# Kernel tuning notes

Hardware: AMD Instinct MI355X
Metric: run time of the kernel (lower is better)

The kernel has to match this reference:

```python
import jax, jax.numpy as jnp
import numpy as np

D_IN, D_H1, D_H2, D_OUT = 24, 64, 128, 64

def setup_inputs() -> dict:
    key = jax.random.key(0)
    ks = jax.random.split(key, 7)
    B, L = 256, 2048
    input_data = jax.random.normal(ks[0], (B, L, D_IN), dtype=jnp.float32)
    s = lambda fan_in: 1.0 / np.sqrt(fan_in)
    W1 = jax.random.uniform(ks[1], (D_IN, D_H1), minval=-s(D_IN), maxval=s(D_IN), dtype=jnp.float32)
    b1 = jax.random.uniform(ks[2], (D_H1,), minval=-s(D_IN), maxval=s(D_IN), dtype=jnp.float32)
    W2 = jax.random.uniform(ks[3], (D_H1, D_H2), minval=-s(D_H1), maxval=s(D_H1), dtype=jnp.float32)
    b2 = jax.random.uniform(ks[4], (D_H2,), minval=-s(D_H1), maxval=s(D_H1), dtype=jnp.float32)
    W3 = jax.random.uniform(ks[5], (D_H2, D_OUT), minval=-s(D_H2), maxval=s(D_H2), dtype=jnp.float32)
    b3 = jax.random.uniform(ks[6], (D_OUT,), minval=-s(D_H2), maxval=s(D_H2), dtype=jnp.float32)
    return {"input_data": input_data, "W1": W1, "b1": b1, "W2": W2, "b2": b2, "W3": W3, "b3": b3, "batch_size": 256}

def reference(input_data, W1, b1, W2, b2, W3, b3, batch_size):
    # Vectorized equivalent of the per-(batch,line) MLP loop:
    # three Linear+ReLU layers applied to every [24]-dim vector.
    h = jax.nn.relu(jnp.einsum('bli,ij->blj', input_data, W1) + b1)
    h = jax.nn.relu(jnp.einsum('bli,ij->blj', h, W2) + b2)
    out = jax.nn.relu(jnp.einsum('bli,ij->blj', h, W3) + b3)  # [B, L, 64]
    return out
```

## Files before the change

### kernel.cpp

```cpp
#include <hip/hip_runtime.h>

typedef float f32x4 __attribute__((ext_vector_type(4)));
typedef short s16x8 __attribute__((ext_vector_type(8)));
typedef unsigned int u32;
typedef unsigned int u32x4 __attribute__((ext_vector_type(4)));
typedef unsigned short u16;

#define DIN 24
#define DH1 64
#define DH2 128
#define DOUT 64

static __device__ __forceinline__ u16 f2bf(float f) {
    u32 u = __builtin_bit_cast(u32, f);
    u += 0x7FFFu + ((u >> 16) & 1u);
    return (u16)(u >> 16);
}
static __device__ __forceinline__ u32 cvtpk(float lo, float hi) {
    u32 r;
    asm("v_cvt_pk_bf16_f32 %0, %1, %2" : "=v"(r) : "v"(lo), "v"(hi));
    return r;
}
static __device__ __forceinline__ float bflo(u32 pk) {
    return __builtin_bit_cast(float, pk << 16);
}
static __device__ __forceinline__ float bfhi(u32 pk) {
    return __builtin_bit_cast(float, pk & 0xFFFF0000u);
}
static __device__ __forceinline__ void swap32(u32& a, u32& b) {
    asm("v_permlane32_swap_b32 %0, %1" : "+v"(a), "+v"(b));
}
static __device__ __forceinline__ void swap16(u32& a, u32& b) {
    asm("v_permlane16_swap_b32 %0, %1" : "+v"(a), "+v"(b));
}

__global__ __launch_bounds__(256, 3) void linenet_r8(
    const float* __restrict__ in,
    const float* __restrict__ W1, const float* __restrict__ b1,
    const float* __restrict__ W2, const float* __restrict__ b2,
    const float* __restrict__ W3, const float* __restrict__ b3,
    float* __restrict__ out, int M)
{
    __shared__ __align__(16) u16 w1lds[4 * 64 * 8];
    __shared__ __align__(16) u16 w2lds[16 * 64 * 8];
    __shared__ __align__(16) u16 w3lds[16 * 64 * 8];

    const int tid  = threadIdx.x;
    const int lane = tid & 63;
    const int gl = lane >> 4, cl = lane & 15;

    {
        const int nt = tid >> 6, ln = tid & 63;
        const int g = ln >> 4, c = ln & 15;
        s16x8 v;
        #pragma unroll
        for (int j = 0; j < 8; ++j) {
            const int k = 8 * g + j;
            u16 x = 0;
            if (k < DIN)       x = f2bf(W1[k * DH1 + nt * 16 + c]);
            else if (k == DIN) x = f2bf(b1[nt * 16 + c]);
            v[j] = (short)x;
        }
        *(s16x8*)&w1lds[tid * 8] = v;
    }
    for (int it = tid; it < 16 * 64; it += 256) {
        const int f = it >> 6, ln = it & 63;
        const int mt = f >> 1, ks = f & 1, g = ln >> 4, c = ln & 15;
        s16x8 v;
        #pragma unroll
        for (int j = 0; j < 8; ++j)
            v[j] = (short)f2bf(W2[(32 * ks + 8 * g + j) * DH2 + mt * 16 + c]);
        *(s16x8*)&w2lds[it * 8] = v;
    }
    for (int it = tid; it < 16 * 64; it += 256) {
        const int f = it >> 6, ln = it & 63;
        const int ks = f >> 2, nt = f & 3, g = ln >> 4, c = ln & 15;
        s16x8 v;
        #pragma unroll
        for (int j = 0; j < 8; ++j)
            v[j] = (short)f2bf(W3[(32 * ks + 8 * g + j) * DOUT + nt * 16 + c]);
        *(s16x8*)&w3lds[it * 8] = v;
    }

    u32 b2pk[8][2], b3pk[4][2];
    #pragma unroll
    for (int mt = 0; mt < 8; ++mt)
        #pragma unroll
        for (int p = 0; p < 2; ++p)
            b2pk[mt][p] = (u32)f2bf(b2[16 * mt + 4 * gl + 2 * p]) |
                          ((u32)f2bf(b2[16 * mt + 4 * gl + 2 * p + 1]) << 16);
    #pragma unroll
    for (int nt = 0; nt < 4; ++nt)
        #pragma unroll
        for (int p = 0; p < 2; ++p)
            b3pk[nt][p] = (u32)f2bf(b3[16 * nt + 4 * gl + 2 * p]) |
                          ((u32)f2bf(b3[16 * nt + 4 * gl + 2 * p + 1]) << 16);

    __syncthreads();

    const int NT = M / 16;
    const int nw = (int)gridDim.x * 4;
    int t = (int)blockIdx.x * 4 + (tid >> 6);
    if (t >= NT) return;

    const int goff = (gl < 3) ? 8 * gl : 0;
    const int loff = cl * DIN + goff;

    f32x4 pf0, pf1;
    {
        const float* p = in + (size_t)t * (16 * DIN) + loff;
        pf0 = *(const f32x4*)p;
        pf1 = *(const f32x4*)(p + 4);
    }

    const f32x4 zac = {0.f, 0.f, 0.f, 0.f};

    while (t < NT) {
        u32x4 aw;
        aw[0] = cvtpk(pf0[0], pf0[1]);
        aw[1] = cvtpk(pf0[2], pf0[3]);
        aw[2] = cvtpk(pf1[0], pf1[1]);
        aw[3] = cvtpk(pf1[2], pf1[3]);
        if (gl == 3) aw[0] = 0x00003F80u;
        const s16x8 a1 = __builtin_bit_cast(s16x8, aw);

        const int tn = t + nw;
        {
            const int tc = (tn < NT) ? tn : t;
            const float* p = in + (size_t)tc * (16 * DIN) + loff;
            pf0 = *(const f32x4*)p;
            pf1 = *(const f32x4*)(p + 4);
        }

        f32x4 acc1[4];
        #pragma unroll
        for (int nt = 0; nt < 4; ++nt) {
            const s16x8 w1f = *(const s16x8*)&w1lds[(nt * 64 + lane) * 8];
            acc1[nt] = __builtin_amdgcn_mfma_f32_16x16x32_bf16(w1f, a1, zac, 0, 0, 0);
        }

        u32 cw[4][2];
        #pragma unroll
        for (int nt = 0; nt < 4; ++nt) {
            cw[nt][0] = cvtpk(fmaxf(acc1[nt][0], 0.f), fmaxf(acc1[nt][1], 0.f));
            cw[nt][1] = cvtpk(fmaxf(acc1[nt][2], 0.f), fmaxf(acc1[nt][3], 0.f));
        }
        swap32(cw[0][0], cw[1][0]); swap32(cw[0][1], cw[1][1]);
        swap32(cw[2][0], cw[3][0]); swap32(cw[2][1], cw[3][1]);
        swap16(cw[0][0], cw[1][0]); swap16(cw[0][1], cw[1][1]);
        swap16(cw[2][0], cw[3][0]); swap16(cw[2][1], cw[3][1]);
        s16x8 bh1[2];
        {
            u32x4 q0 = {cw[0][0], cw[0][1], cw[1][0], cw[1][1]};
            u32x4 q1 = {cw[2][0], cw[2][1], cw[3][0], cw[3][1]};
            bh1[0] = __builtin_bit_cast(s16x8, q0);
            bh1[1] = __builtin_bit_cast(s16x8, q1);
        }

        u32 cw2[8][2];
        #pragma unroll
        for (int mt = 0; mt < 8; ++mt) {
            f32x4 c2;
            c2[0] = bflo(b2pk[mt][0]); c2[1] = bfhi(b2pk[mt][0]);
            c2[2] = bflo(b2pk[mt][1]); c2[3] = bfhi(b2pk[mt][1]);
            const s16x8 w2a = *(const s16x8*)&w2lds[((mt * 2 + 0) * 64 + lane) * 8];
            const s16x8 w2b = *(const s16x8*)&w2lds[((mt * 2 + 1) * 64 + lane) * 8];
            f32x4 acc2 = __builtin_amdgcn_mfma_f32_16x16x32_bf16(w2a, bh1[0], c2, 0, 0, 0);
            acc2 = __builtin_amdgcn_mfma_f32_16x16x32_bf16(w2b, bh1[1], acc2, 0, 0, 0);
            cw2[mt][0] = cvtpk(fmaxf(acc2[0], 0.f), fmaxf(acc2[1], 0.f));
            cw2[mt][1] = cvtpk(fmaxf(acc2[2], 0.f), fmaxf(acc2[3], 0.f));
        }
        #pragma unroll
        for (int m = 0; m < 8; m += 2) {
            swap32(cw2[m][0], cw2[m + 1][0]);
            swap32(cw2[m][1], cw2[m + 1][1]);
        }
        #pragma unroll
        for (int m = 0; m < 8; m += 2) {
            swap16(cw2[m][0], cw2[m + 1][0]);
            swap16(cw2[m][1], cw2[m + 1][1]);
        }
        s16x8 bh2[4];
        #pragma unroll
        for (int ks = 0; ks < 4; ++ks) {
            u32x4 q = {cw2[2 * ks][0], cw2[2 * ks][1],
                       cw2[2 * ks + 1][0], cw2[2 * ks + 1][1]};
            bh2[ks] = __builtin_bit_cast(s16x8, q);
        }

        f32x4 acc3[4];
        #pragma unroll
        for (int nt = 0; nt < 4; ++nt) {
            acc3[nt][0] = bflo(b3pk[nt][0]); acc3[nt][1] = bfhi(b3pk[nt][0]);
            acc3[nt][2] = bflo(b3pk[nt][1]); acc3[nt][3] = bfhi(b3pk[nt][1]);
        }
        #pragma unroll
        for (int ks = 0; ks < 4; ++ks) {
            #pragma unroll
            for (int nt = 0; nt < 4; ++nt) {
                const s16x8 wf = *(const s16x8*)&w3lds[((ks * 4 + nt) * 64 + lane) * 8];
                acc3[nt] = __builtin_amdgcn_mfma_f32_16x16x32_bf16(
                    wf, bh2[ks], acc3[nt], 0, 0, 0);
            }
        }

        float* const ob = out + (size_t)t * (16 * DOUT) + (size_t)cl * DOUT;
        #pragma unroll
        for (int nt = 0; nt < 4; ++nt) {
            f32x4 v;
            v[0] = fmaxf(acc3[nt][0], 0.f); v[1] = fmaxf(acc3[nt][1], 0.f);
            v[2] = fmaxf(acc3[nt][2], 0.f); v[3] = fmaxf(acc3[nt][3], 0.f);
            *(f32x4*)&ob[16 * nt + 4 * gl] = v;
        }

        t = tn;
    }
}

extern "C" void kernel_launch(void* const* d_in, const int* in_sizes, int n_in,
                              void* d_out, int out_size, void* d_ws, size_t ws_size,
                              hipStream_t stream)
{
    const float* in = (const float*)d_in[0];
    const float* W1 = (const float*)d_in[1];
    const float* b1 = (const float*)d_in[2];
    const float* W2 = (const float*)d_in[3];
    const float* b2 = (const float*)d_in[4];
    const float* W3 = (const float*)d_in[5];
    const float* b3 = (const float*)d_in[6];
    float* out = (float*)d_out;
    const int M = in_sizes[0] / DIN;

    dim3 grid(768), block(256);
    hipLaunchKernelGGL(linenet_r8, grid, block, 0, stream,
                       in, W1, b1, W2, b2, W3, b3, out, M);
}
```

Baseline: 40.23 us.

## Process two row tiles per wave iteration to share weight fragment loads

Each wave now handles two 16-row tiles per loop iteration, interleaving their MFMA chains so every LDS weight fragment read feeds two MFMAs and independent chains hide MFMA latency. Input prefetch is doubled to cover both tiles. To fit the extra registers, launch bounds drop to 2 blocks per CU and the grid shrinks from 768 to 512 blocks. This trades occupancy for instruction-level parallelism and halved LDS traffic per tile.

```diff
diff --git a/kernel.cpp b/kernel.cpp
--- a/kernel.cpp
+++ b/kernel.cpp
@@ -34,7 +34,7 @@
     asm("v_permlane16_swap_b32 %0, %1" : "+v"(a), "+v"(b));
 }
 
-__global__ __launch_bounds__(256, 3) void linenet_r8(
+__global__ __launch_bounds__(256, 2) void linenet_r10(
     const float* __restrict__ in,
     const float* __restrict__ W1, const float* __restrict__ b1,
     const float* __restrict__ W2, const float* __restrict__ b2,
@@ -106,58 +106,76 @@
     const int goff = (gl < 3) ? 8 * gl : 0;
     const int loff = cl * DIN + goff;
 
-    f32x4 pf0, pf1;
+    f32x4 pfA0, pfA1, pfB0, pfB1;
     {
         const float* p = in + (size_t)t * (16 * DIN) + loff;
-        pf0 = *(const f32x4*)p;
-        pf1 = *(const f32x4*)(p + 4);
+        pfA0 = *(const f32x4*)p; pfA1 = *(const f32x4*)(p + 4);
+        const int tB = (t + nw < NT) ? t + nw : t;
+        const float* q = in + (size_t)tB * (16 * DIN) + loff;
+        pfB0 = *(const f32x4*)q; pfB1 = *(const f32x4*)(q + 4);
     }
 
     const f32x4 zac = {0.f, 0.f, 0.f, 0.f};
 
     while (t < NT) {
-        u32x4 aw;
-        aw[0] = cvtpk(pf0[0], pf0[1]);
-        aw[1] = cvtpk(pf0[2], pf0[3]);
-        aw[2] = cvtpk(pf1[0], pf1[1]);
-        aw[3] = cvtpk(pf1[2], pf1[3]);
-        if (gl == 3) aw[0] = 0x00003F80u;
-        const s16x8 a1 = __builtin_bit_cast(s16x8, aw);
-
-        const int tn = t + nw;
+        const int tB = (t + nw < NT) ? t + nw : t;
+
+        u32x4 awA, awB;
+        awA[0] = cvtpk(pfA0[0], pfA0[1]); awA[1] = cvtpk(pfA0[2], pfA0[3]);
+        awA[2] = cvtpk(pfA1[0], pfA1[1]); awA[3] = cvtpk(pfA1[2], pfA1[3]);
+        awB[0] = cvtpk(pfB0[0], pfB0[1]); awB[1] = cvtpk(pfB0[2], pfB0[3]);
+        awB[2] = cvtpk(pfB1[0], pfB1[1]); awB[3] = cvtpk(pfB1[2], pfB1[3]);
+        if (gl == 3) { awA[0] = 0x00003F80u; awB[0] = 0x00003F80u; }
+        const s16x8 a1A = __builtin_bit_cast(s16x8, awA);
+        const s16x8 a1B = __builtin_bit_cast(s16x8, awB);
+
+        const int tn = t + 2 * nw;
         {
-            const int tc = (tn < NT) ? tn : t;
+            const int tc  = (tn < NT) ? tn : t;
+            const int tcB = (tn + nw < NT) ? tn + nw : tc;
             const float* p = in + (size_t)tc * (16 * DIN) + loff;
-            pf0 = *(const f32x4*)p;
-            pf1 = *(const f32x4*)(p + 4);
-        }
-
-        f32x4 acc1[4];
+            pfA0 = *(const f32x4*)p; pfA1 = *(const f32x4*)(p + 4);
+            const float* q = in + (size_t)tcB * (16 * DIN) + loff;
+            pfB0 = *(const f32x4*)q; pfB1 = *(const f32x4*)(q + 4);
+        }
+
+        f32x4 accA1[4], accB1[4];
         #pragma unroll
         for (int nt = 0; nt < 4; ++nt) {
             const s16x8 w1f = *(const s16x8*)&w1lds[(nt * 64 + lane) * 8];
-            acc1[nt] = __builtin_amdgcn_mfma_f32_16x16x32_bf16(w1f, a1, zac, 0, 0, 0);
-        }
-
-        u32 cw[4][2];
-        #pragma unroll
-        for (int nt = 0; nt < 4; ++nt) {
-            cw[nt][0] = cvtpk(fmaxf(acc1[nt][0], 0.f), fmaxf(acc1[nt][1], 0.f));
-            cw[nt][1] = cvtpk(fmaxf(acc1[nt][2], 0.f), fmaxf(acc1[nt][3], 0.f));
-        }
-        swap32(cw[0][0], cw[1][0]); swap32(cw[0][1], cw[1][1]);
-        swap32(cw[2][0], cw[3][0]); swap32(cw[2][1], cw[3][1]);
-        swap16(cw[0][0], cw[1][0]); swap16(cw[0][1], cw[1][1]);
-        swap16(cw[2][0], cw[3][0]); swap16(cw[2][1], cw[3][1]);
-        s16x8 bh1[2];
+            accA1[nt] = __builtin_amdgcn_mfma_f32_16x16x32_bf16(w1f, a1A, zac, 0, 0, 0);
+            accB1[nt] = __builtin_amdgcn_mfma_f32_16x16x32_bf16(w1f, a1B, zac, 0, 0, 0);
+        }
+
+        u32 cwA[4][2], cwB[4][2];
+        #pragma unroll
+        for (int nt = 0; nt < 4; ++nt) {
+            cwA[nt][0] = cvtpk(fmaxf(accA1[nt][0], 0.f), fmaxf(accA1[nt][1], 0.f));
+            cwA[nt][1] = cvtpk(fmaxf(accA1[nt][2], 0.f), fmaxf(accA1[nt][3], 0.f));
+            cwB[nt][0] = cvtpk(fmaxf(accB1[nt][0], 0.f), fmaxf(accB1[nt][1], 0.f));
+            cwB[nt][1] = cvtpk(fmaxf(accB1[nt][2], 0.f), fmaxf(accB1[nt][3], 0.f));
+        }
+        swap32(cwA[0][0], cwA[1][0]); swap32(cwA[0][1], cwA[1][1]);
+        swap32(cwA[2][0], cwA[3][0]); swap32(cwA[2][1], cwA[3][1]);
+        swap16(cwA[0][0], cwA[1][0]); swap16(cwA[0][1], cwA[1][1]);
+        swap16(cwA[2][0], cwA[3][0]); swap16(cwA[2][1], cwA[3][1]);
+        swap32(cwB[0][0], cwB[1][0]); swap32(cwB[0][1], cwB[1][1]);
+        swap32(cwB[2][0], cwB[3][0]); swap32(cwB[2][1], cwB[3][1]);
+        swap16(cwB[0][0], cwB[1][0]); swap16(cwB[0][1], cwB[1][1]);
+        swap16(cwB[2][0], cwB[3][0]); swap16(cwB[2][1], cwB[3][1]);
+        s16x8 bh1A[2], bh1B[2];
         {
-            u32x4 q0 = {cw[0][0], cw[0][1], cw[1][0], cw[1][1]};
-            u32x4 q1 = {cw[2][0], cw[2][1], cw[3][0], cw[3][1]};
-            bh1[0] = __builtin_bit_cast(s16x8, q0);
-            bh1[1] = __builtin_bit_cast(s16x8, q1);
-        }
-
-        u32 cw2[8][2];
+            u32x4 q0 = {cwA[0][0], cwA[0][1], cwA[1][0], cwA[1][1]};
+            u32x4 q1 = {cwA[2][0], cwA[2][1], cwA[3][0], cwA[3][1]};
+            bh1A[0] = __builtin_bit_cast(s16x8, q0);
+            bh1A[1] = __builtin_bit_cast(s16x8, q1);
+            u32x4 r0 = {cwB[0][0], cwB[0][1], cwB[1][0], cwB[1][1]};
+            u32x4 r1 = {cwB[2][0], cwB[2][1], cwB[3][0], cwB[3][1]};
+            bh1B[0] = __builtin_bit_cast(s16x8, r0);
+            bh1B[1] = __builtin_bit_cast(s16x8, r1);
+        }
+
+        u32 cw2A[8][2], cw2B[8][2];
         #pragma unroll
         for (int mt = 0; mt < 8; ++mt) {
             f32x4 c2;
@@ -165,55 +183,72 @@
             c2[2] = bflo(b2pk[mt][1]); c2[3] = bfhi(b2pk[mt][1]);
             const s16x8 w2a = *(const s16x8*)&w2lds[((mt * 2 + 0) * 64 + lane) * 8];
             const s16x8 w2b = *(const s16x8*)&w2lds[((mt * 2 + 1) * 64 + lane) * 8];
-            f32x4 acc2 = __builtin_amdgcn_mfma_f32_16x16x32_bf16(w2a, bh1[0], c2, 0, 0, 0);
-            acc2 = __builtin_amdgcn_mfma_f32_16x16x32_bf16(w2b, bh1[1], acc2, 0, 0, 0);
-            cw2[mt][0] = cvtpk(fmaxf(acc2[0], 0.f), fmaxf(acc2[1], 0.f));
-            cw2[mt][1] = cvtpk(fmaxf(acc2[2], 0.f), fmaxf(acc2[3], 0.f));
+            f32x4 aA = __builtin_amdgcn_mfma_f32_16x16x32_bf16(w2a, bh1A[0], c2, 0, 0, 0);
+            f32x4 aB = __builtin_amdgcn_mfma_f32_16x16x32_bf16(w2a, bh1B[0], c2, 0, 0, 0);
+            aA = __builtin_amdgcn_mfma_f32_16x16x32_bf16(w2b, bh1A[1], aA, 0, 0, 0);
+            aB = __builtin_amdgcn_mfma_f32_16x16x32_bf16(w2b, bh1B[1], aB, 0, 0, 0);
+            cw2A[mt][0] = cvtpk(fmaxf(aA[0], 0.f), fmaxf(aA[1], 0.f));
+            cw2A[mt][1] = cvtpk(fmaxf(aA[2], 0.f), fmaxf(aA[3], 0.f));
+            cw2B[mt][0] = cvtpk(fmaxf(aB[0], 0.f), fmaxf(aB[1], 0.f));
+            cw2B[mt][1] = cvtpk(fmaxf(aB[2], 0.f), fmaxf(aB[3], 0.f));
         }
         #pragma unroll
         for (int m = 0; m < 8; m += 2) {
-            swap32(cw2[m][0], cw2[m + 1][0]);
-            swap32(cw2[m][1], cw2[m + 1][1]);
+            swap32(cw2A[m][0], cw2A[m + 1][0]); swap32(cw2A[m][1], cw2A[m + 1][1]);
+            swap32(cw2B[m][0], cw2B[m + 1][0]); swap32(cw2B[m][1], cw2B[m + 1][1]);
         }
         #pragma unroll
         for (int m = 0; m < 8; m += 2) {
-            swap16(cw2[m][0], cw2[m + 1][0]);
-            swap16(cw2[m][1], cw2[m + 1][1]);
-        }
-        s16x8 bh2[4];
+            swap16(cw2A[m][0], cw2A[m + 1][0]); swap16(cw2A[m][1], cw2A[m + 1][1]);
+            swap16(cw2B[m][0], cw2B[m + 1][0]); swap16(cw2B[m][1], cw2B[m + 1][1]);
+        }
+        s16x8 bh2A[4], bh2B[4];
         #pragma unroll
         for (int ks = 0; ks < 4; ++ks) {
-            u32x4 q = {cw2[2 * ks][0], cw2[2 * ks][1],
-                       cw2[2 * ks + 1][0], cw2[2 * ks + 1][1]};
-            bh2[ks] = __builtin_bit_cast(s16x8, q);
-        }
-
-        f32x4 acc3[4];
-        #pragma unroll
-        for (int nt = 0; nt < 4; ++nt) {
-            acc3[nt][0] = bflo(b3pk[nt][0]); acc3[nt][1] = bfhi(b3pk[nt][0]);
-            acc3[nt][2] = bflo(b3pk[nt][1]); acc3[nt][3] = bfhi(b3pk[nt][1]);
+            u32x4 q = {cw2A[2 * ks][0], cw2A[2 * ks][1],
+                       cw2A[2 * ks + 1][0], cw2A[2 * ks + 1][1]};
+            bh2A[ks] = __builtin_bit_cast(s16x8, q);
+            u32x4 r = {cw2B[2 * ks][0], cw2B[2 * ks][1],
+                       cw2B[2 * ks + 1][0], cw2B[2 * ks + 1][1]};
+            bh2B[ks] = __builtin_bit_cast(s16x8, r);
+        }
+
+        f32x4 accA3[4], accB3[4];
+        #pragma unroll
+        for (int nt = 0; nt < 4; ++nt) {
+            f32x4 c3;
+            c3[0] = bflo(b3pk[nt][0]); c3[1] = bfhi(b3pk[nt][0]);
+            c3[2] = bflo(b3pk[nt][1]); c3[3] = bfhi(b3pk[nt][1]);
+            accA3[nt] = c3; accB3[nt] = c3;
         }
         #pragma unroll
         for (int ks = 0; ks < 4; ++ks) {
             #pragma unroll
             for (int nt = 0; nt < 4; ++nt) {
                 const s16x8 wf = *(const s16x8*)&w3lds[((ks * 4 + nt) * 64 + lane) * 8];
-                acc3[nt] = __builtin_amdgcn_mfma_f32_16x16x32_bf16(
-                    wf, bh2[ks], acc3[nt], 0, 0, 0);
+                accA3[nt] = __builtin_amdgcn_mfma_f32_16x16x32_bf16(wf, bh2A[ks], accA3[nt], 0, 0, 0);
+                accB3[nt] = __builtin_amdgcn_mfma_f32_16x16x32_bf16(wf, bh2B[ks], accB3[nt], 0, 0, 0);
             }
         }
 
-        float* const ob = out + (size_t)t * (16 * DOUT) + (size_t)cl * DOUT;
+        float* const obA = out + (size_t)t  * (16 * DOUT) + (size_t)cl * DOUT;
+        float* const obB = out + (size_t)tB * (16 * DOUT) + (size_t)cl * DOUT;
         #pragma unroll
         for (int nt = 0; nt < 4; ++nt) {
             f32x4 v;
-            v[0] = fmaxf(acc3[nt][0], 0.f); v[1] = fmaxf(acc3[nt][1], 0.f);
-            v[2] = fmaxf(acc3[nt][2], 0.f); v[3] = fmaxf(acc3[nt][3], 0.f);
-            *(f32x4*)&ob[16 * nt + 4 * gl] = v;
-        }
-
-        t = tn;
+            v[0] = fmaxf(accA3[nt][0], 0.f); v[1] = fmaxf(accA3[nt][1], 0.f);
+            v[2] = fmaxf(accA3[nt][2], 0.f); v[3] = fmaxf(accA3[nt][3], 0.f);
+            *(f32x4*)&obA[16 * nt + 4 * gl] = v;
+        }
+        #pragma unroll
+        for (int nt = 0; nt < 4; ++nt) {
+            f32x4 v;
+            v[0] = fmaxf(accB3[nt][0], 0.f); v[1] = fmaxf(accB3[nt][1], 0.f);
+            v[2] = fmaxf(accB3[nt][2], 0.f); v[3] = fmaxf(accB3[nt][3], 0.f);
+            *(f32x4*)&obB[16 * nt + 4 * gl] = v;
+        }
+
+        t += 2 * nw;
     }
 }
 
@@ -231,7 +266,7 @@
     float* out = (float*)d_out;
     const int M = in_sizes[0] / DIN;
 
-    dim3 grid(768), block(256);
-    hipLaunchKernelGGL(linenet_r8, grid, block, 0, stream,
+    dim3 grid(512), block(256);
+    hipLaunchKernelGGL(linenet_r10, grid, block, 0, stream,
                        in, W1, b1, W2, b2, W3, b3, out, M);
 }
```

After: 40.87 us. No clear change (+1.6%).
